# Optimization experiments

Hardware: AMD Instinct MI355X
Metric: run time of the kernel (lower is better)

## Reference

```python
import jax, jax.numpy as jnp
import numpy as np

B, T, F, CI, CO, K, DIL = 16, 512, 32, 128, 128, 3, 2


def setup_inputs() -> dict:
    key = jax.random.key(0)
    k1, k2, k3 = jax.random.split(key, 3)
    x = jax.random.normal(k1, (B, T, F, CI), dtype=jnp.float32)
    # torch Conv1d weight per feature: [CO, CI, K]; stack over features -> [F, CO, CI, K]
    fan_in = CI * K
    bound = 1.0 / np.sqrt(fan_in)
    w = jax.random.uniform(k2, (F, CO, CI, K), dtype=jnp.float32, minval=-bound, maxval=bound)
    b = jax.random.uniform(k3, (F, CO), dtype=jnp.float32, minval=-bound, maxval=bound)
    return {"x": x, "w": w, "b": b}


def reference(x, w, b):
    # Causal dilated conv, independent filters per feature.
    left_pad = DIL * (K - 1)
    xpad = jnp.pad(x, ((0, 0), (left_pad, 0), (0, 0), (0, 0)))  # [B, T+L, F, CI]
    # taps[k] = xpad[:, k*DIL : k*DIL + T] -> stack over kernel taps: [K, B, T, F, CI]
    taps = jnp.stack([xpad[:, k * DIL:k * DIL + T] for k in range(K)], axis=0)
    # y[b,t,f,o] = sum_{k,i} taps[k,b,t,f,i] * w[f,o,i,k] + b[f,o]
    y = jnp.einsum('kbtfi,foik->btfo', taps, w) + b[None, None, :, :]
    return y  # dropout p=0.0 (eval) is identity
```

## Files before the change

kernel.cpp:

```cpp
#include <hip/hip_runtime.h>
#include <stdint.h>

#define B_ 16
#define T_ 512
#define F_ 32
#define CI_ 128
#define CO_ 128
#define K_ 3
#define LPAD 4
#define TM 64
#define XROWS (TM + LPAD)
#define XPITCH 136
#define WPITCH 32
#define CHUNK_ELEMS (CO_ * WPITCH)
#define NCHUNK 12

typedef __attribute__((ext_vector_type(8))) __bf16 bf16x8;
typedef __attribute__((ext_vector_type(4))) float f32x4;

__device__ __forceinline__ uint16_t f2bf(float x) {
  uint32_t u = __builtin_bit_cast(uint32_t, x);
  u += 0x7fffu + ((u >> 16) & 1u);
  return (uint16_t)(u >> 16);
}

__global__ __launch_bounds__(256) void repack_w(const float* __restrict__ w,
                                                uint16_t* __restrict__ wt2) {
  int idx = blockIdx.x * 256 + threadIdx.x;
  int i = idx & (CI_ - 1);
  int fo = idx >> 7;
  int o = fo & (CO_ - 1);
  int f = fo >> 7;
  const float* src = w + (size_t)idx * K_;
  float a0 = src[0], a1 = src[1], a2 = src[2];
  size_t base = ((size_t)f * NCHUNK + (i >> 5)) * CHUNK_ELEMS + o * WPITCH + (i & 31);
  wt2[base] = f2bf(a0);
  wt2[base + 4 * (size_t)CHUNK_ELEMS] = f2bf(a1);
  wt2[base + 8 * (size_t)CHUNK_ELEMS] = f2bf(a2);
}

template <bool PACKED>
__global__ __launch_bounds__(256, 4) void conv_main(
    const float* __restrict__ x, const uint16_t* __restrict__ wt2,
    const float* __restrict__ wraw, const float* __restrict__ bias,
    float* __restrict__ y) {
  __shared__ __align__(16) uint16_t xs[XROWS * XPITCH];
  __shared__ __align__(16) uint16_t wbuf[2][CHUNK_ELEMS];

  const int bid = blockIdx.x;
  const int f = bid >> 7;
  const int mt = bid & 127;
  const int b = mt >> 3;
  const int t0 = (mt & 7) << 6;

  const int tid = threadIdx.x;
  const int lane = tid & 63;
  const int wave = tid >> 6;
  const int wm = wave >> 1;
  const int wn = wave & 1;
  const int l15 = lane & 15;
  const int quad = lane >> 4;

  f32x4 acc[2][4];
#pragma unroll
  for (int fn = 0; fn < 4; ++fn) {
    float bv = bias[f * CO_ + wn * 64 + fn * 16 + l15];
#pragma unroll
    for (int fm = 0; fm < 2; ++fm) acc[fm][fn] = (f32x4){bv, bv, bv, bv};
  }

  auto issue_chunk = [&](int idx, int buf) {
    const uint16_t* src = wt2 + ((size_t)(f * NCHUNK + idx)) * CHUNK_ELEMS;
    for (int c = wave; c < 8; c += 4)
      __builtin_amdgcn_global_load_lds(
          (const __attribute__((address_space(1))) uint32_t*)(src + c * 512 + lane * 8),
          (__attribute__((address_space(3))) uint32_t*)&wbuf[buf][c * 512], 16, 0, 0);
  };
  auto gather_chunk = [&](int idx, int buf) {
    int tap = idx >> 2, i0 = (idx & 3) << 5;
    for (int e = tid; e < CHUNK_ELEMS; e += 256) {
      int o = e >> 5, i = i0 + (e & 31);
      wbuf[buf][e] = f2bf(wraw[(((size_t)(f * CO_ + o)) * CI_ + i) * K_ + tap]);
    }
  };

  if constexpr (PACKED) issue_chunk(0, 0);

  {
    const float* xb = x + ((size_t)b * T_ * F_ + f) * CI_;
    for (int idx = tid; idx < XROWS * 32; idx += 256) {
      int row = idx >> 5, c4 = idx & 31;
      int t = t0 - LPAD + row;
      float4 v = make_float4(0.f, 0.f, 0.f, 0.f);
      if (t >= 0) v = *(const float4*)(xb + (size_t)t * (F_ * CI_) + c4 * 4);
      uint2 pk;
      pk.x = (uint32_t)f2bf(v.x) | ((uint32_t)f2bf(v.y) << 16);
      pk.y = (uint32_t)f2bf(v.z) | ((uint32_t)f2bf(v.w) << 16);
      *(uint2*)&xs[row * XPITCH + c4 * 4] = pk;
    }
  }
  if constexpr (!PACKED) gather_chunk(0, 0);
  __syncthreads();

#pragma unroll 1
  for (int idx = 0; idx < NCHUNK; ++idx) {
    const int cur = idx & 1;
    if (idx + 1 < NCHUNK) {
      if constexpr (PACKED) issue_chunk(idx + 1, cur ^ 1);
      else gather_chunk(idx + 1, cur ^ 1);
    }

    const int tap = idx >> 2;
    const int kq0 = (idx & 3) * 32 + quad * 8;
    const int xr0 = wm * 32 + l15 + 2 * tap;
    bf16x8 av[2], bv[4];
#pragma unroll
    for (int fm = 0; fm < 2; ++fm)
      av[fm] = *(const bf16x8*)&xs[(xr0 + fm * 16) * XPITCH + kq0];
#pragma unroll
    for (int fn = 0; fn < 4; ++fn)
      bv[fn] = *(const bf16x8*)&wbuf[cur][(wn * 64 + fn * 16 + l15) * WPITCH + quad * 8];
#pragma unroll
    for (int fm = 0; fm < 2; ++fm)
#pragma unroll
      for (int fn = 0; fn < 4; ++fn)
        acc[fm][fn] = __builtin_amdgcn_mfma_f32_16x16x32_bf16(av[fm], bv[fn],
                                                              acc[fm][fn], 0, 0, 0);
    if (idx + 1 < NCHUNK) __syncthreads();
  }

  float* yb = y + ((size_t)b * T_ * F_ + f) * CO_;
#pragma unroll
  for (int fm = 0; fm < 2; ++fm) {
    int r0 = t0 + wm * 32 + fm * 16 + quad * 4;
#pragma unroll
    for (int fn = 0; fn < 4; ++fn) {
      int col = wn * 64 + fn * 16 + l15;
#pragma unroll
      for (int r = 0; r < 4; ++r)
        yb[(size_t)(r0 + r) * (F_ * CO_) + col] = acc[fm][fn][r];
    }
  }
}

extern "C" void kernel_launch(void* const* d_in, const int* in_sizes, int n_in,
                              void* d_out, int out_size, void* d_ws, size_t ws_size,
                              hipStream_t stream) {
  const float* x = (const float*)d_in[0];
  const float* w = (const float*)d_in[1];
  const float* bias = (const float*)d_in[2];
  float* y = (float*)d_out;

  const size_t wt2_bytes = (size_t)F_ * NCHUNK * CHUNK_ELEMS * sizeof(uint16_t);
  const int main_blocks = F_ * B_ * (T_ / TM);

  if (ws_size >= wt2_bytes) {
    uint16_t* wt2 = (uint16_t*)d_ws;
    const int total = F_ * CO_ * CI_;
    repack_w<<<total / 256, 256, 0, stream>>>(w, wt2);
    conv_main<true><<<main_blocks, 256, 0, stream>>>(x, wt2, w, bias, y);
  } else {
    conv_main<false><<<main_blocks, 256, 0, stream>>>(x, (const uint16_t*)nullptr, w, bias, y);
  }
}
```

Baseline: 278.9 us.

## Keep per-feature weights in registers and loop over time tiles per block

Each block now covers one (feature, batch) pair across all eight time tiles with 512 threads. Each wave holds its 16-output-channel slice of the bf16 weights in registers for the whole block, so weights are no longer staged through LDS and reloaded once per time tile. The next x tile is prefetched into registers while the current one is computed, then converted to bf16 in LDS. The grid shrinks from 4096 blocks to 512, which may reduce parallelism and latency hiding. Register pressure also rises from the 12 resident weight vectors plus the prefetch buffers.

Result: faster. 267.4 us (-4.1%).

```diff
diff --git a/kernel.cpp b/kernel.cpp
--- a/kernel.cpp
+++ b/kernel.cpp
@@ -14,6 +14,7 @@
 #define WPITCH 32
 #define CHUNK_ELEMS (CO_ * WPITCH)
 #define NCHUNK 12
+#define NXV 5
 
 typedef __attribute__((ext_vector_type(8))) __bf16 bf16x8;
 typedef __attribute__((ext_vector_type(4))) float f32x4;
@@ -40,105 +41,107 @@
 }
 
 template <bool PACKED>
-__global__ __launch_bounds__(256, 4) void conv_main(
+__global__ __launch_bounds__(512, 4) void conv_main(
     const float* __restrict__ x, const uint16_t* __restrict__ wt2,
     const float* __restrict__ wraw, const float* __restrict__ bias,
     float* __restrict__ y) {
   __shared__ __align__(16) uint16_t xs[XROWS * XPITCH];
-  __shared__ __align__(16) uint16_t wbuf[2][CHUNK_ELEMS];
 
   const int bid = blockIdx.x;
-  const int f = bid >> 7;
-  const int mt = bid & 127;
-  const int b = mt >> 3;
-  const int t0 = (mt & 7) << 6;
+  const int f = bid >> 4;
+  const int b = bid & 15;
 
   const int tid = threadIdx.x;
   const int lane = tid & 63;
   const int wave = tid >> 6;
-  const int wm = wave >> 1;
-  const int wn = wave & 1;
   const int l15 = lane & 15;
   const int quad = lane >> 4;
+  const int co0 = wave * 16;
 
-  f32x4 acc[2][4];
+  bf16x8 wreg[NCHUNK];
+  if constexpr (PACKED) {
+    const uint16_t* wp = wt2 + (size_t)f * NCHUNK * CHUNK_ELEMS + (co0 + l15) * WPITCH + quad * 8;
 #pragma unroll
-  for (int fn = 0; fn < 4; ++fn) {
-    float bv = bias[f * CO_ + wn * 64 + fn * 16 + l15];
+    for (int c = 0; c < NCHUNK; ++c)
+      wreg[c] = *(const bf16x8*)(wp + c * CHUNK_ELEMS);
+  } else {
 #pragma unroll
-    for (int fm = 0; fm < 2; ++fm) acc[fm][fn] = (f32x4){bv, bv, bv, bv};
+    for (int c = 0; c < NCHUNK; ++c) {
+      int tap = c >> 2, i0 = (c & 3) * 32 + quad * 8;
+      const float* ws = wraw + (((size_t)(f * CO_ + co0 + l15)) * CI_ + i0) * K_ + tap;
+      union { bf16x8 v; uint16_t h[8]; } u;
+#pragma unroll
+      for (int j = 0; j < 8; ++j) u.h[j] = f2bf(ws[j * K_]);
+      wreg[c] = u.v;
+    }
   }
+  const float bv = bias[f * CO_ + co0 + l15];
 
-  auto issue_chunk = [&](int idx, int buf) {
-    const uint16_t* src = wt2 + ((size_t)(f * NCHUNK + idx)) * CHUNK_ELEMS;
-    for (int c = wave; c < 8; c += 4)
-      __builtin_amdgcn_global_load_lds(
-          (const __attribute__((address_space(1))) uint32_t*)(src + c * 512 + lane * 8),
-          (__attribute__((address_space(3))) uint32_t*)&wbuf[buf][c * 512], 16, 0, 0);
+  const float* xb = x + ((size_t)b * T_ * F_ + f) * CI_;
+  float4 xr[NXV];
+
+  auto load_x = [&](int t0) {
+#pragma unroll
+    for (int it = 0; it < NXV; ++it) {
+      int idx = tid + it * 512;
+      if (idx < XROWS * 32) {
+        int row = idx >> 5, c4 = idx & 31;
+        int t = t0 - LPAD + row;
+        xr[it] = (t >= 0) ? *(const float4*)(xb + (size_t)t * (F_ * CI_) + c4 * 4)
+                          : make_float4(0.f, 0.f, 0.f, 0.f);
+      }
+    }
   };
-  auto gather_chunk = [&](int idx, int buf) {
-    int tap = idx >> 2, i0 = (idx & 3) << 5;
-    for (int e = tid; e < CHUNK_ELEMS; e += 256) {
-      int o = e >> 5, i = i0 + (e & 31);
-      wbuf[buf][e] = f2bf(wraw[(((size_t)(f * CO_ + o)) * CI_ + i) * K_ + tap]);
+  auto store_x = [&]() {
+#pragma unroll
+    for (int it = 0; it < NXV; ++it) {
+      int idx = tid + it * 512;
+      if (idx < XROWS * 32) {
+        int row = idx >> 5, c4 = idx & 31;
+        uint2 pk;
+        pk.x = (uint32_t)f2bf(xr[it].x) | ((uint32_t)f2bf(xr[it].y) << 16);
+        pk.y = (uint32_t)f2bf(xr[it].z) | ((uint32_t)f2bf(xr[it].w) << 16);
+        *(uint2*)&xs[row * XPITCH + c4 * 4] = pk;
+      }
     }
   };
 
-  if constexpr (PACKED) issue_chunk(0, 0);
-
-  {
-    const float* xb = x + ((size_t)b * T_ * F_ + f) * CI_;
-    for (int idx = tid; idx < XROWS * 32; idx += 256) {
-      int row = idx >> 5, c4 = idx & 31;
-      int t = t0 - LPAD + row;
-      float4 v = make_float4(0.f, 0.f, 0.f, 0.f);
-      if (t >= 0) v = *(const float4*)(xb + (size_t)t * (F_ * CI_) + c4 * 4);
-      uint2 pk;
-      pk.x = (uint32_t)f2bf(v.x) | ((uint32_t)f2bf(v.y) << 16);
-      pk.y = (uint32_t)f2bf(v.z) | ((uint32_t)f2bf(v.w) << 16);
-      *(uint2*)&xs[row * XPITCH + c4 * 4] = pk;
-    }
-  }
-  if constexpr (!PACKED) gather_chunk(0, 0);
+  load_x(0);
+  store_x();
+  load_x(TM);
   __syncthreads();
 
+  const int abase = l15 * XPITCH + quad * 8;
+
 #pragma unroll 1
-  for (int idx = 0; idx < NCHUNK; ++idx) {
-    const int cur = idx & 1;
-    if (idx + 1 < NCHUNK) {
-      if constexpr (PACKED) issue_chunk(idx + 1, cur ^ 1);
-      else gather_chunk(idx + 1, cur ^ 1);
+  for (int j = 0; j < 8; ++j) {
+    const int t0 = j * TM;
+    f32x4 acc[4];
+#pragma unroll
+    for (int fm = 0; fm < 4; ++fm) acc[fm] = (f32x4){bv, bv, bv, bv};
+
+#pragma unroll
+    for (int c = 0; c < NCHUNK; ++c) {
+      const int tap = c >> 2, ks = c & 3;
+#pragma unroll
+      for (int fm = 0; fm < 4; ++fm) {
+        bf16x8 av = *(const bf16x8*)&xs[abase + (2 * tap + fm * 16) * XPITCH + ks * 32];
+        acc[fm] = __builtin_amdgcn_mfma_f32_16x16x32_bf16(av, wreg[c], acc[fm], 0, 0, 0);
+      }
     }
 
-    const int tap = idx >> 2;
-    const int kq0 = (idx & 3) * 32 + quad * 8;
-    const int xr0 = wm * 32 + l15 + 2 * tap;
-    bf16x8 av[2], bv[4];
+    float* yb = y + (((size_t)b * T_ + t0) * F_ + f) * CO_ + co0;
 #pragma unroll
-    for (int fm = 0; fm < 2; ++fm)
-      av[fm] = *(const bf16x8*)&xs[(xr0 + fm * 16) * XPITCH + kq0];
-#pragma unroll
-    for (int fn = 0; fn < 4; ++fn)
-      bv[fn] = *(const bf16x8*)&wbuf[cur][(wn * 64 + fn * 16 + l15) * WPITCH + quad * 8];
-#pragma unroll
-    for (int fm = 0; fm < 2; ++fm)
-#pragma unroll
-      for (int fn = 0; fn < 4; ++fn)
-        acc[fm][fn] = __builtin_amdgcn_mfma_f32_16x16x32_bf16(av[fm], bv[fn],
-                                                              acc[fm][fn], 0, 0, 0);
-    if (idx + 1 < NCHUNK) __syncthreads();
-  }
-
-  float* yb = y + ((size_t)b * T_ * F_ + f) * CO_;
-#pragma unroll
-  for (int fm = 0; fm < 2; ++fm) {
-    int r0 = t0 + wm * 32 + fm * 16 + quad * 4;
-#pragma unroll
-    for (int fn = 0; fn < 4; ++fn) {
-      int col = wn * 64 + fn * 16 + l15;
+    for (int fm = 0; fm < 4; ++fm)
 #pragma unroll
       for (int r = 0; r < 4; ++r)
-        yb[(size_t)(r0 + r) * (F_ * CO_) + col] = acc[fm][fn][r];
+        yb[(size_t)(fm * 16 + quad * 4 + r) * (F_ * CO_) + l15] = acc[fm][r];
+
+    if (j < 7) {
+      __syncthreads();
+      store_x();
+      if (j < 6) load_x((j + 2) * TM);
+      __syncthreads();
     }
   }
 }
@@ -152,14 +155,14 @@
   float* y = (float*)d_out;
 
   const size_t wt2_bytes = (size_t)F_ * NCHUNK * CHUNK_ELEMS * sizeof(uint16_t);
-  const int main_blocks = F_ * B_ * (T_ / TM);
+  const int main_blocks = F_ * B_;
 
   if (ws_size >= wt2_bytes) {
     uint16_t* wt2 = (uint16_t*)d_ws;
     const int total = F_ * CO_ * CI_;
     repack_w<<<total / 256, 256, 0, stream>>>(w, wt2);
-    conv_main<true><<<main_blocks, 256, 0, stream>>>(x, wt2, w, bias, y);
+    conv_main<true><<<main_blocks, 512, 0, stream>>>(x, wt2, w, bias, y);
   } else {
-    conv_main<false><<<main_blocks, 256, 0, stream>>>(x, (const uint16_t*)nullptr, w, bias, y);
+    conv_main<false><<<main_blocks, 512, 0, stream>>>(x, (const uint16_t*)nullptr, w, bias, y);
   }
 }
```
